# Performance work log

Measured on AMD Instinct MI355X. Metric: run time of the kernel, lower is better.

## Reference

```python
import jax, jax.numpy as jnp
import numpy as np

WORD_VOCAB = 100000
TAG_VOCAB = 60
DW = 300   # word embed dim
DT = 50    # tag embed dim
H = 300    # hidden size
DEPTH = 13
N_NODES = 2 ** DEPTH - 1      # 8191
N_LEAVES = 2 ** (DEPTH - 1)   # 4096


def setup_inputs() -> dict:
    key = jax.random.key(0)
    ks = jax.random.split(key, 10)
    scale = 0.05
    return {
        "leaf_word_ids": jax.random.randint(ks[0], (N_LEAVES,), 0, WORD_VOCAB, dtype=jnp.int32),
        # tag ids laid out level-by-level, leaves first, root last
        "tag_ids": jax.random.randint(ks[1], (N_NODES,), 0, TAG_VOCAB, dtype=jnp.int32),
        "word_table": jax.random.normal(ks[2], (WORD_VOCAB, DW), jnp.float32) * scale,
        "tag_table": jax.random.normal(ks[3], (TAG_VOCAB, DT), jnp.float32) * scale,
        "Wr": jax.random.normal(ks[4], (DW + DT + 2 * H, H), jnp.float32) * scale,
        "br": jnp.zeros((H,), jnp.float32),
        "Wz": jax.random.normal(ks[5], (DW + DT + 2 * H, H), jnp.float32) * scale,
        "bz": jnp.zeros((H,), jnp.float32),
        "Wu": jax.random.normal(ks[6], (DW + 2 * H, H), jnp.float32) * scale,
        "bu": jnp.zeros((H,), jnp.float32),
    }


def reference(leaf_word_ids, tag_ids, word_table, tag_table, Wr, br, Wz, bz, Wu, bu):
    """Labeled binary tree GRU over a complete binary tree, batched by depth.

    Leaves (which carry words) are processed first with zero child states,
    then each internal level combines adjacent child pairs, exactly the
    per-node math of LabeledBinaryTreeGRU.node_forward.
    """
    h_dim = Wr.shape[1]
    dw = word_table.shape[1]
    dtype = word_table.dtype

    def gru(we, te, lh, rh):
        # we:[m,DW] te:[m,DT] lh,rh:[m,H]
        x = jnp.concatenate([we, te, lh, rh], axis=1)
        r = jax.nn.sigmoid(x @ Wr + br)
        z = jax.nn.sigmoid(x @ Wz + bz)
        u = jnp.tanh(jnp.concatenate([we, r * lh, r * rh], axis=1) @ Wu + bu)
        return z * (lh + rh) + (1.0 - z) * u

    n_leaf = leaf_word_ids.shape[0]
    # leaf level: real word embeddings, zero child states
    we = word_table[leaf_word_ids]
    te = tag_table[tag_ids[:n_leaf]]
    zeros_h = jnp.zeros((n_leaf, h_dim), dtype)
    h = gru(we, te, zeros_h, zeros_h)
    outputs = [h]

    off = n_leaf
    m = n_leaf // 2
    while m >= 1:
        lh = h[0::2]   # left children of this level's parents
        rh = h[1::2]   # right children
        te = tag_table[tag_ids[off:off + m]]
        we = jnp.zeros((m, dw), dtype)  # internal nodes have no word (node.idx is None)
        h = gru(we, te, lh, rh)
        outputs.append(h)
        off += m
        m //= 2

    outputs = jnp.concatenate(outputs, axis=0)  # [N_NODES, H]
    final_state = h                              # [1, H] root state
    return outputs, final_state
```

## Files before the change

### kernel.cpp

```cpp
#include <hip/hip_runtime.h>
#include <math.h>

#define H 300
#define NLEAF 4096

typedef unsigned int  uint;
typedef unsigned short ushort;
typedef __attribute__((ext_vector_type(8))) short  short8;
typedef __attribute__((ext_vector_type(4))) float  f32x4;

__device__ __forceinline__ float sigmoidf_(float x) { return 1.0f / (1.0f + expf(-x)); }

__device__ __forceinline__ ushort f2bf(float f)
{
    uint u = __float_as_uint(f);
    u += 0x7FFF + ((u >> 16) & 1);
    return (ushort)(u >> 16);
}
__device__ __forceinline__ uint2 pack4(float4 v)
{
    uint2 w;
    w.x = (uint)f2bf(v.x) | ((uint)f2bf(v.y) << 16);
    w.y = (uint)f2bf(v.z) | ((uint)f2bf(v.w) << 16);
    return w;
}

template<int NT, int KSTEPS, int KT, int AS>
__device__ __forceinline__ void mfma_gemm(const ushort* A_lds, const ushort* __restrict__ Bt,
                                          int tile0, int s0, int lane, f32x4* acc)
{
    const ushort* Ap = A_lds + (lane & 15) * AS + ((lane >> 4) * 8) + s0 * 32;
    const ushort* Bp[NT];
    #pragma unroll
    for (int t = 0; t < NT; ++t)
        Bp[t] = Bt + ((long)(tile0 + t) * KT + s0) * 512 + lane * 8;

    short8 aA, aB, bA[NT], bB[NT];
    aA = *(const short8*)Ap;
    #pragma unroll
    for (int t = 0; t < NT; ++t) bA[t] = *(const short8*)Bp[t];

    int s = 0;
    #pragma unroll 1
    for (; s + 2 < KSTEPS; s += 2) {
        aB = *(const short8*)(Ap + (s + 1) * 32);
        #pragma unroll
        for (int t = 0; t < NT; ++t) bB[t] = *(const short8*)(Bp[t] + (s + 1) * 512);
        #pragma unroll
        for (int t = 0; t < NT; ++t)
            acc[t] = __builtin_amdgcn_mfma_f32_16x16x32_bf16(aA, bA[t], acc[t], 0, 0, 0);
        aA = *(const short8*)(Ap + (s + 2) * 32);
        #pragma unroll
        for (int t = 0; t < NT; ++t) bA[t] = *(const short8*)(Bp[t] + (s + 2) * 512);
        #pragma unroll
        for (int t = 0; t < NT; ++t)
            acc[t] = __builtin_amdgcn_mfma_f32_16x16x32_bf16(aB, bB[t], acc[t], 0, 0, 0);
    }
    if (KSTEPS - s == 2) {
        aB = *(const short8*)(Ap + (s + 1) * 32);
        #pragma unroll
        for (int t = 0; t < NT; ++t) bB[t] = *(const short8*)(Bp[t] + (s + 1) * 512);
        #pragma unroll
        for (int t = 0; t < NT; ++t)
            acc[t] = __builtin_amdgcn_mfma_f32_16x16x32_bf16(aA, bA[t], acc[t], 0, 0, 0);
        #pragma unroll
        for (int t = 0; t < NT; ++t)
            acc[t] = __builtin_amdgcn_mfma_f32_16x16x32_bf16(aB, bB[t], acc[t], 0, 0, 0);
    } else {
        #pragma unroll
        for (int t = 0; t < NT; ++t)
            acc[t] = __builtin_amdgcn_mfma_f32_16x16x32_bf16(aA, bA[t], acc[t], 0, 0, 0);
    }
}

__global__ __launch_bounds__(256) void prep_k(
    const float* __restrict__ Wr, const float* __restrict__ Wz,
    const float* __restrict__ Wu, const float* __restrict__ tag_table,
    const float* __restrict__ br, const float* __restrict__ bz,
    ushort* __restrict__ WArzT, ushort* __restrict__ WuTpT, ushort* __restrict__ WLzuT,
    float* __restrict__ tag_r, float* __restrict__ tag_z)
{
    __shared__ float te[50];
    int b = blockIdx.x;
    int tid = threadIdx.x;
    if (b < 640) {
        int c = b;
        int tile = c >> 4, cl = c & 15;
        int gate = (c >= 320);
        int cc = gate ? c - 320 : c;
        const float* WA = gate ? Wz : Wr;
        for (int o = tid; o < 76; o += 256) {
            int k0 = o * 8;
            ushort tmp[8];
            #pragma unroll
            for (int i = 0; i < 8; ++i) {
                int k = k0 + i;
                float v = 0.f;
                if (cc < 300) {
                    if (k < 300) v = WA[(350 + k) * H + cc];
                    else if (k >= 304 && k < 604) v = WA[(k + 346) * H + cc];
                }
                tmp[i] = f2bf(v);
            }
            int s = k0 >> 5, kk0 = k0 & 31;
            long pos = ((long)(tile * 19 + s)) * 512 + ((kk0 >> 3) * 16 + cl) * 8;
            uint4 w;
            w.x = (uint)tmp[0] | ((uint)tmp[1] << 16);
            w.y = (uint)tmp[2] | ((uint)tmp[3] << 16);
            w.z = (uint)tmp[4] | ((uint)tmp[5] << 16);
            w.w = (uint)tmp[6] | ((uint)tmp[7] << 16);
            *(uint4*)&WArzT[pos] = w;
        }
        const float* WL = gate ? Wu : Wz;
        for (int o = tid; o < 40; o += 256) {
            int k0 = o * 8;
            ushort tmp[8];
            #pragma unroll
            for (int i = 0; i < 8; ++i) {
                int k = k0 + i;
                float v = (cc < 300 && k < 300) ? WL[k * H + cc] : 0.f;
                tmp[i] = f2bf(v);
            }
            int s = k0 >> 5, kk0 = k0 & 31;
            long pos = ((long)(tile * 10 + s)) * 512 + ((kk0 >> 3) * 16 + cl) * 8;
            uint4 w;
            w.x = (uint)tmp[0] | ((uint)tmp[1] << 16);
            w.y = (uint)tmp[2] | ((uint)tmp[3] << 16);
            w.z = (uint)tmp[4] | ((uint)tmp[5] << 16);
            w.w = (uint)tmp[6] | ((uint)tmp[7] << 16);
            *(uint4*)&WLzuT[pos] = w;
        }
        if (c < 320) {
            for (int o = tid; o < 76; o += 256) {
                int k0 = o * 8;
                ushort tmp[8];
                #pragma unroll
                for (int i = 0; i < 8; ++i) {
                    int k = k0 + i;
                    float v = 0.f;
                    if (c < 300) {
                        if (k < 300) v = Wu[(300 + k) * H + c];
                        else if (k >= 304 && k < 604) v = Wu[(k + 296) * H + c];
                    }
                    tmp[i] = f2bf(v);
                }
                int s = k0 >> 5, kk0 = k0 & 31;
                long pos = ((long)(tile * 19 + s)) * 512 + ((kk0 >> 3) * 16 + cl) * 8;
                uint4 w;
                w.x = (uint)tmp[0] | ((uint)tmp[1] << 16);
                w.y = (uint)tmp[2] | ((uint)tmp[3] << 16);
                w.z = (uint)tmp[4] | ((uint)tmp[5] << 16);
                w.w = (uint)tmp[6] | ((uint)tmp[7] << 16);
                *(uint4*)&WuTpT[pos] = w;
            }
        }
    } else {
        int t = b - 640;
        if (tid < 50) te[tid] = tag_table[t * 50 + tid];
        __syncthreads();
        for (int k = tid; k < H; k += 256) {
            float ar = br[k], az = bz[k];
            #pragma unroll 10
            for (int j = 0; j < 50; ++j) {
                float tv = te[j];
                ar = fmaf(tv, Wr[(H + j) * H + k], ar);
                az = fmaf(tv, Wz[(H + j) * H + k], az);
            }
            tag_r[t * H + k] = ar;
            tag_z[t * H + k] = az;
        }
    }
}

__global__ __launch_bounds__(512, 1) void leaf_mfma_k(
    const int* __restrict__ word_ids, const int* __restrict__ tag_ids,
    const float* __restrict__ word_table, const ushort* __restrict__ WLzuT,
    const float* __restrict__ bu, const float* __restrict__ tag_z,
    float* __restrict__ out)
{
    __shared__ ushort Abf[16 * 328];
    __shared__ float zbuf[16][304];
    int tid = threadIdx.x;
    int node0 = blockIdx.x * 16;

    for (int idx = tid; idx < 16 * 82; idx += 512) {
        int j = idx / 82, q = idx - j * 82;
        char* rowb = (char*)(Abf + j * 328);
        if (q < 75) {
            float4 v = ((const float4*)(word_table + (long)word_ids[node0 + j] * H))[q];
            *(uint2*)(rowb + q * 8) = pack4(v);
        } else {
            *(uint2*)(rowb + q * 8) = make_uint2(0u, 0u);
        }
    }
    __syncthreads();

    int wv = tid >> 6, lane = tid & 63;
    int jrow = (lane >> 4) * 4;

    f32x4 acc[5];
    #pragma unroll
    for (int t = 0; t < 5; ++t) acc[t] = (f32x4)(0.f);

    if (wv < 4) {
        mfma_gemm<5, 10, 10, 328>(Abf, WLzuT, wv * 5, 0, lane, acc);
        int tg[4];
        #pragma unroll
        for (int q = 0; q < 4; ++q) tg[q] = tag_ids[node0 + jrow + q];
        #pragma unroll
        for (int t = 0; t < 5; ++t) {
            int c = wv * 80 + t * 16 + (lane & 15);
            #pragma unroll
            for (int q = 0; q < 4; ++q)
                if (c < 300) zbuf[jrow + q][c] = sigmoidf_(acc[t][q] + tag_z[tg[q] * H + c]);
        }
    } else {
        mfma_gemm<5, 10, 10, 328>(Abf, WLzuT, 20 + (wv - 4) * 5, 0, lane, acc);
    }
    __syncthreads();
    if (wv >= 4) {
        #pragma unroll
        for (int t = 0; t < 5; ++t) {
            int c = (wv - 4) * 80 + t * 16 + (lane & 15);
            #pragma unroll
            for (int q = 0; q < 4; ++q) {
                if (c < 300) {
                    int jn = jrow + q;
                    float u = tanhf(acc[t][q] + bu[c]);
                    out[(long)(node0 + jn) * H + c] = (1.f - zbuf[jn][c]) * u;
                }
            }
        }
    }
}

__device__ __forceinline__ void fused_body(
    const int* __restrict__ tag_ids, const ushort* __restrict__ WArzT,
    const ushort* __restrict__ WuTpT, const float* __restrict__ bu,
    const float* __restrict__ tag_r, const float* __restrict__ tag_z,
    float* __restrict__ out, int off, int prevOff, int m, float* __restrict__ dup,
    int node0, int tid, ushort* Abf, float (*zbuf)[304], float (*pbuf)[64][21])
{
    for (int idx = tid; idx < 16 * 154; idx += 512) {
        int j = idx / 154, q = idx - j * 154;
        char* rowb = (char*)(Abf + j * 616);
        bool valid = (node0 + j) < m;
        if (q < 75) {
            uint2 w = make_uint2(0u, 0u);
            if (valid) {
                float4 v = ((const float4*)(out + (long)(prevOff + 2 * (node0 + j)) * H))[q];
                w = pack4(v);
            }
            *(uint2*)(rowb + q * 8) = w;
        } else if (q < 150) {
            int qq = q - 75;
            uint2 w = make_uint2(0u, 0u);
            if (valid) {
                float4 v = ((const float4*)(out + (long)(prevOff + 2 * (node0 + j) + 1) * H))[qq];
                w = pack4(v);
            }
            *(uint2*)(rowb + 608 + qq * 8) = w;
        } else {
            int pb = (q == 150) ? 600 : (1208 + (q - 151) * 8);
            *(uint2*)(rowb + pb) = make_uint2(0u, 0u);
        }
    }
    __syncthreads();

    int wv = tid >> 6, lane = tid & 63;
    int jrow = (lane >> 4) * 4;
    int tg[4];
    #pragma unroll
    for (int q = 0; q < 4; ++q) {
        int gn = node0 + jrow + q;
        tg[q] = tag_ids[off + (gn < m ? gn : 0)];
    }

    f32x4 accG[5];
    #pragma unroll
    for (int t = 0; t < 5; ++t) accG[t] = (f32x4)(0.f);
    mfma_gemm<5, 19, 19, 616>(Abf, WArzT, wv * 5, 0, lane, accG);
    __syncthreads();

    float Sr[5][4];
    if (wv < 4) {
        #pragma unroll
        for (int t = 0; t < 5; ++t) {
            int c = wv * 80 + t * 16 + (lane & 15);
            #pragma unroll
            for (int q = 0; q < 4; ++q) {
                int jn = jrow + q, gn = node0 + jn;
                if (c < 300 && gn < m) {
                    float lh = out[(long)(prevOff + 2 * gn) * H + c];
                    float rh = out[(long)(prevOff + 2 * gn + 1) * H + c];
                    float r  = sigmoidf_(accG[t][q] + tag_r[tg[q] * H + c]);
                    Sr[t][q] = lh + rh;
                    Abf[jn * 616 + c]       = f2bf(r * lh);
                    Abf[jn * 616 + 304 + c] = f2bf(r * rh);
                }
            }
        }
    } else {
        #pragma unroll
        for (int t = 0; t < 5; ++t) {
            int cz = (wv - 4) * 80 + t * 16 + (lane & 15);
            #pragma unroll
            for (int q = 0; q < 4; ++q) {
                int jn = jrow + q, gn = node0 + jn;
                if (cz < 300 && gn < m)
                    zbuf[jn][cz] = sigmoidf_(accG[t][q] + tag_z[tg[q] * H + cz]);
            }
        }
    }
    __syncthreads();

    f32x4 accU[5];
    #pragma unroll
    for (int t = 0; t < 5; ++t) accU[t] = (f32x4)(0.f);
    if (wv < 4) {
        mfma_gemm<5, 10, 19, 616>(Abf, WuTpT, wv * 5, 0, lane, accU);
    } else {
        mfma_gemm<5, 9, 19, 616>(Abf, WuTpT, (wv - 4) * 5, 10, lane, accU);
        #pragma unroll
        for (int t = 0; t < 5; ++t)
            #pragma unroll
            for (int q = 0; q < 4; ++q)
                pbuf[wv - 4][lane][t * 4 + q] = accU[t][q];
    }
    __syncthreads();
    if (wv < 4) {
        #pragma unroll
        for (int t = 0; t < 5; ++t) {
            int c = wv * 80 + t * 16 + (lane & 15);
            #pragma unroll
            for (int q = 0; q < 4; ++q) {
                int jn = jrow + q, gn = node0 + jn;
                if (c < 300 && gn < m) {
                    float a = accU[t][q] + pbuf[wv][lane][t * 4 + q];
                    float u = tanhf(a + bu[c]);
                    float z = zbuf[jn][c];
                    float h = z * Sr[t][q] + (1.f - z) * u;
                    out[(long)(off + gn) * H + c] = h;
                    if (dup && gn == 0) dup[c] = h;
                }
            }
        }
    }
}

__global__ __launch_bounds__(512, 1) void level_fused_k(
    const int* __restrict__ tag_ids, const ushort* __restrict__ WArzT,
    const ushort* __restrict__ WuTpT, const float* __restrict__ bu,
    const float* __restrict__ tag_r, const float* __restrict__ tag_z,
    float* __restrict__ out, int off, int prevOff, int m)
{
    __shared__ ushort Abf[16 * 616];
    __shared__ float zbuf[16][304];
    __shared__ float pbuf[4][64][21];
    fused_body(tag_ids, WArzT, WuTpT, bu, tag_r, tag_z, out, off, prevOff, m,
               nullptr, blockIdx.x * 16, threadIdx.x, Abf, zbuf, pbuf);
}

__global__ __launch_bounds__(512, 1) void tail4_k(
    const int* __restrict__ tag_ids, const ushort* __restrict__ WArzT,
    const ushort* __restrict__ WuTpT, const float* __restrict__ bu,
    const float* __restrict__ tag_r, const float* __restrict__ tag_z,
    float* __restrict__ out, float* __restrict__ finalDup)
{
    __shared__ ushort Abf[16 * 616];
    __shared__ float zbuf[16][304];
    __shared__ float pbuf[4][64][21];
    int off = 8176, prevOff = 8160;
    for (int m = 8; m >= 1; m >>= 1) {
        fused_body(tag_ids, WArzT, WuTpT, bu, tag_r, tag_z, out, off, prevOff, m,
                   (m == 1) ? finalDup : nullptr, 0, threadIdx.x, Abf, zbuf, pbuf);
        __syncthreads();
        prevOff = off;
        off += m;
    }
}

extern "C" void kernel_launch(void* const* d_in, const int* in_sizes, int n_in,
                              void* d_out, int out_size, void* d_ws, size_t ws_size,
                              hipStream_t stream)
{
    const int*   word_ids   = (const int*)  d_in[0];
    const int*   tag_ids    = (const int*)  d_in[1];
    const float* word_table = (const float*)d_in[2];
    const float* tag_table  = (const float*)d_in[3];
    const float* Wr         = (const float*)d_in[4];
    const float* br         = (const float*)d_in[5];
    const float* Wz         = (const float*)d_in[6];
    const float* bz         = (const float*)d_in[7];
    const float* Wu         = (const float*)d_in[8];
    const float* bu         = (const float*)d_in[9];
    float* out = (float*)d_out;

    float* tag_r = (float*)d_ws;
    float* tag_z = tag_r + 18000;
    ushort* WArzT = (ushort*)(tag_z + 18000);
    ushort* WuTpT = WArzT + 40L * 19 * 512;
    ushort* WLzuT = WuTpT + 20L * 19 * 512;

    prep_k<<<700, 256, 0, stream>>>(Wr, Wz, Wu, tag_table, br, bz,
                                    WArzT, WuTpT, WLzuT, tag_r, tag_z);

    leaf_mfma_k<<<NLEAF / 16, 512, 0, stream>>>(
        word_ids, tag_ids, word_table, WLzuT, bu, tag_z, out);

    int off = NLEAF, prevOff = 0;
    for (int m = 2048; m >= 16; m >>= 1) {
        level_fused_k<<<m / 16, 512, 0, stream>>>(
            tag_ids, WArzT, WuTpT, bu, tag_r, tag_z, out, off, prevOff, m);
        prevOff = off;
        off += m;
    }

    float* finalDup = out + (long)8191 * H;
    tail4_k<<<1, 512, 0, stream>>>(
        tag_ids, WArzT, WuTpT, bu, tag_r, tag_z, out, finalDup);
}
```

Baseline: 279.2 us.

## Deepen MFMA operand prefetch ring and fold the m=16 level into tail kernel

Replaces the two-stage double-buffered A/B operand loads in the MFMA GEMM helper with a fully unrolled ring of up to four in-flight k-steps, so more loads are outstanding while each MFMA runs. Separately, the level with 16 nodes moves from a separate single-block launch into the persistent tail kernel, removing one kernel launch. The deeper ring raises VGPR pressure, and the single-block tail now serially does one more level.

```diff
diff --git a/kernel.cpp b/kernel.cpp
--- a/kernel.cpp
+++ b/kernel.cpp
@@ -35,41 +35,27 @@
     for (int t = 0; t < NT; ++t)
         Bp[t] = Bt + ((long)(tile0 + t) * KT + s0) * 512 + lane * 8;
 
-    short8 aA, aB, bA[NT], bB[NT];
-    aA = *(const short8*)Ap;
-    #pragma unroll
-    for (int t = 0; t < NT; ++t) bA[t] = *(const short8*)Bp[t];
-
-    int s = 0;
-    #pragma unroll 1
-    for (; s + 2 < KSTEPS; s += 2) {
-        aB = *(const short8*)(Ap + (s + 1) * 32);
-        #pragma unroll
-        for (int t = 0; t < NT; ++t) bB[t] = *(const short8*)(Bp[t] + (s + 1) * 512);
+    constexpr int D = (KSTEPS < 4) ? KSTEPS : 4;
+    short8 aP[D];
+    short8 bP[D][NT];
+    #pragma unroll
+    for (int i = 0; i < D; ++i) {
+        aP[i] = *(const short8*)(Ap + i * 32);
+        #pragma unroll
+        for (int t = 0; t < NT; ++t) bP[i][t] = *(const short8*)(Bp[t] + i * 512);
+    }
+    #pragma unroll
+    for (int s = 0; s < KSTEPS; ++s) {
+        const int slot = s % D;
         #pragma unroll
         for (int t = 0; t < NT; ++t)
-            acc[t] = __builtin_amdgcn_mfma_f32_16x16x32_bf16(aA, bA[t], acc[t], 0, 0, 0);
-        aA = *(const short8*)(Ap + (s + 2) * 32);
-        #pragma unroll
-        for (int t = 0; t < NT; ++t) bA[t] = *(const short8*)(Bp[t] + (s + 2) * 512);
-        #pragma unroll
-        for (int t = 0; t < NT; ++t)
-            acc[t] = __builtin_amdgcn_mfma_f32_16x16x32_bf16(aB, bB[t], acc[t], 0, 0, 0);
-    }
-    if (KSTEPS - s == 2) {
-        aB = *(const short8*)(Ap + (s + 1) * 32);
-        #pragma unroll
-        for (int t = 0; t < NT; ++t) bB[t] = *(const short8*)(Bp[t] + (s + 1) * 512);
-        #pragma unroll
-        for (int t = 0; t < NT; ++t)
-            acc[t] = __builtin_amdgcn_mfma_f32_16x16x32_bf16(aA, bA[t], acc[t], 0, 0, 0);
-        #pragma unroll
-        for (int t = 0; t < NT; ++t)
-            acc[t] = __builtin_amdgcn_mfma_f32_16x16x32_bf16(aB, bB[t], acc[t], 0, 0, 0);
-    } else {
-        #pragma unroll
-        for (int t = 0; t < NT; ++t)
-            acc[t] = __builtin_amdgcn_mfma_f32_16x16x32_bf16(aA, bA[t], acc[t], 0, 0, 0);
+            acc[t] = __builtin_amdgcn_mfma_f32_16x16x32_bf16(aP[slot], bP[slot][t], acc[t], 0, 0, 0);
+        if (s + D < KSTEPS) {
+            aP[slot] = *(const short8*)(Ap + (s + D) * 32);
+            #pragma unroll
+            for (int t = 0; t < NT; ++t)
+                bP[slot][t] = *(const short8*)(Bp[t] + (s + D) * 512);
+        }
     }
 }
 
@@ -361,7 +347,7 @@
                nullptr, blockIdx.x * 16, threadIdx.x, Abf, zbuf, pbuf);
 }
 
-__global__ __launch_bounds__(512, 1) void tail4_k(
+__global__ __launch_bounds__(512, 1) void tail5_k(
     const int* __restrict__ tag_ids, const ushort* __restrict__ WArzT,
     const ushort* __restrict__ WuTpT, const float* __restrict__ bu,
     const float* __restrict__ tag_r, const float* __restrict__ tag_z,
@@ -370,8 +356,8 @@
     __shared__ ushort Abf[16 * 616];
     __shared__ float zbuf[16][304];
     __shared__ float pbuf[4][64][21];
-    int off = 8176, prevOff = 8160;
-    for (int m = 8; m >= 1; m >>= 1) {
+    int off = 8160, prevOff = 8128;
+    for (int m = 16; m >= 1; m >>= 1) {
         fused_body(tag_ids, WArzT, WuTpT, bu, tag_r, tag_z, out, off, prevOff, m,
                    (m == 1) ? finalDup : nullptr, 0, threadIdx.x, Abf, zbuf, pbuf);
         __syncthreads();
@@ -409,7 +395,7 @@
         word_ids, tag_ids, word_table, WLzuT, bu, tag_z, out);
 
     int off = NLEAF, prevOff = 0;
-    for (int m = 2048; m >= 16; m >>= 1) {
+    for (int m = 2048; m >= 32; m >>= 1) {
         level_fused_k<<<m / 16, 512, 0, stream>>>(
             tag_ids, WArzT, WuTpT, bu, tag_r, tag_z, out, off, prevOff, m);
         prevOff = off;
@@ -417,6 +403,6 @@
     }
 
     float* finalDup = out + (long)8191 * H;
-    tail4_k<<<1, 512, 0, stream>>>(
+    tail5_k<<<1, 512, 0, stream>>>(
         tag_ids, WArzT, WuTpT, bu, tag_r, tag_z, out, finalDup);
 }
```

After: 388.8 us. +39.3%, slower.
